# Kernel tuning notes

Hardware: AMD Instinct MI355X
Metric: run time of the kernel (lower is better)

The kernel has to match this reference:

```python
import jax, jax.numpy as jnp
import numpy as np

N_NODES = 50000
DEGREE = 32
NUM_FEATS = 128
NUM_HIDDEN = 128
NUM_LABELS = 40


def setup_inputs() -> dict:
    key = jax.random.key(0)
    k1, k2, k3, k4, k5, k6 = jax.random.split(key, 6)
    feats = jax.random.normal(k1, (N_NODES, NUM_FEATS), dtype=jnp.float32)
    neigh = jax.random.randint(k2, (N_NODES, DEGREE), 0, N_NODES, dtype=jnp.int32)
    batch = jnp.arange(N_NODES, dtype=jnp.int32)
    s1 = 1.0 / np.sqrt(2 * NUM_FEATS)
    s2 = 1.0 / np.sqrt(2 * NUM_HIDDEN)
    W1 = jax.random.uniform(k3, (2 * NUM_FEATS, NUM_HIDDEN), jnp.float32, -s1, s1)
    b1 = jax.random.uniform(k4, (NUM_HIDDEN,), jnp.float32, -s1, s1)
    W2 = jax.random.uniform(k5, (2 * NUM_HIDDEN, NUM_LABELS), jnp.float32, -s2, s2)
    b2 = jax.random.uniform(k6, (NUM_LABELS,), jnp.float32, -s2, s2)
    return {"feats": feats, "neigh": neigh, "batch": batch,
            "W1": W1, "b1": b1, "W2": W2, "b2": b2}


def reference(feats, neigh, batch, W1, b1, W2, b2):
    # Layer 1 (GraphConvolution with mean aggregator, relu; dropout in eval mode = identity).
    # Compute gc1 embeddings for ALL nodes once: identical math to the per-node
    # Python loop since the mean aggregator is deterministic.
    nbr_mean1 = jnp.take(feats, neigh, axis=0).mean(axis=1)          # [N, F]
    z1 = jnp.concatenate([feats, nbr_mean1], axis=-1)                # [N, 2F]
    h1 = jax.nn.relu(z1 @ W1 + b1)                                   # [N, H]
    # Layer 2 (no activation): concat self embedding with mean of neighbor embeddings.
    nbr_mean2 = jnp.take(h1, neigh[batch], axis=0).mean(axis=1)      # [B, H]
    z2 = jnp.concatenate([h1[batch], nbr_mean2], axis=-1)            # [B, 2H]
    return z2 @ W2 + b2                                              # [B, L]
```

## Files before the change

### kernel.cpp

```cpp
#include <hip/hip_runtime.h>
#include <hip/hip_bf16.h>

typedef __attribute__((ext_vector_type(8))) short short8;
typedef __attribute__((ext_vector_type(4))) float f32x4;

#define NFEAT 128
#define DEG 32
#define FSCALE 24.0f
#define FDEC (1.0f / (24.0f * 32.0f))
#define YSCALE 64.0f
#define YDEC (1.0f / (64.0f * 32.0f))

static __device__ __forceinline__ unsigned short f2bf(float f) {
    unsigned u = __float_as_uint(f);
    u += 0x7fffu + ((u >> 16) & 1u);
    return (unsigned short)(u >> 16);
}
static __device__ __forceinline__ int sxt8(unsigned x) {
    return (int)(signed char)(x & 0xffu);
}

__global__ void prep_all_kernel(const float* __restrict__ feats,
                                unsigned short* __restrict__ featsb,
                                unsigned* __restrict__ feats8,
                                const float* __restrict__ W1,
                                unsigned short* __restrict__ W1p,
                                const float* __restrict__ W2,
                                unsigned short* __restrict__ W2p,
                                int n4, int nPrepBlocks, int L) {
    int b = blockIdx.x;
    if (b < nPrepBlocks) {
        int i = b * 256 + threadIdx.x;
        if (i < n4) {
            float4 f = ((const float4*)feats)[i];
            ushort4 ob;
            ob.x = f2bf(f.x); ob.y = f2bf(f.y); ob.z = f2bf(f.z); ob.w = f2bf(f.w);
            ((ushort4*)featsb)[i] = ob;
            int a0 = max(-127, min(127, __float2int_rn(f.x * FSCALE)));
            int a1 = max(-127, min(127, __float2int_rn(f.y * FSCALE)));
            int a2 = max(-127, min(127, __float2int_rn(f.z * FSCALE)));
            int a3 = max(-127, min(127, __float2int_rn(f.w * FSCALE)));
            feats8[i] = (unsigned)(a0 & 0xff) | ((unsigned)(a1 & 0xff) << 8) |
                        ((unsigned)(a2 & 0xff) << 16) | ((unsigned)(a3 & 0xff) << 24);
        }
    } else if (b < nPrepBlocks + 128) {
        int t = (b - nPrepBlocks) * 256 + threadIdx.x;
        int j    = t & 7;
        int lane = (t >> 3) & 63;
        int ks   = (t >> 9) & 7;
        int nt   = t >> 12;
        int k    = ks * 32 + (lane >> 4) * 8 + j;
        int col  = nt * 16 + (lane & 15);
        W1p[t] = f2bf(W1[k * 128 + col]);
    } else {
        int t = (b - nPrepBlocks - 128) * 256 + threadIdx.x;
        if (t < 7 * 4 * 64 * 8) {
            int j    = t & 7;
            int lane = (t >> 3) & 63;
            int ks   = (t >> 9) & 3;
            int nt   = t >> 11;
            int k    = ks * 32 + (lane >> 4) * 8 + j;
            int p    = nt * 16 + (lane & 15);
            float v = 0.f;
            if (p < 48) { if (p < L) v = W2[k * L + p]; }
            else        { int cc = p - 48; if (cc < L) v = W2[(128 + k) * L + cc]; }
            W2p[t] = f2bf(v);
        }
    }
}

__global__ __launch_bounds__(256, 4) void layer1_fused_kernel(
    const unsigned short* __restrict__ tableb,
    const unsigned char* __restrict__ table8,
    const int* __restrict__ neigh,
    const unsigned short* __restrict__ W1p,
    const float* __restrict__ b1,
    const unsigned short* __restrict__ W2p,
    const float* __restrict__ b2,
    float* __restrict__ X2,
    signed char* __restrict__ Y2,
    int nRows, int L)
{
    __shared__ unsigned int z1[16 * 128];
    const int tid = threadIdx.x;
    const int w = tid >> 6;
    const int l = tid & 63;
    const int jg = l >> 3;
    const int c = l & 7;

    int srow = tid >> 4, sch = tid & 15;
    int sr = min(blockIdx.x * 16 + srow, nRows - 1);
    uint4 selfv = ((const uint4*)(tableb + (size_t)sr * NFEAT))[sch];

    const int r0 = blockIdx.x * 16 + w * 4;
    const int* nbp0 = neigh + (size_t)min(r0 + 0, nRows - 1) * DEG;
    const int* nbp1 = neigh + (size_t)min(r0 + 1, nRows - 1) * DEG;
    const int* nbp2 = neigh + (size_t)min(r0 + 2, nRows - 1) * DEG;
    const int* nbp3 = neigh + (size_t)min(r0 + 3, nRows - 1) * DEG;
    int i00 = nbp0[jg], i01 = nbp0[8 + jg], i02 = nbp0[16 + jg], i03 = nbp0[24 + jg];
    int i10 = nbp1[jg], i11 = nbp1[8 + jg], i12 = nbp1[16 + jg], i13 = nbp1[24 + jg];
    int i20 = nbp2[jg], i21 = nbp2[8 + jg], i22 = nbp2[16 + jg], i23 = nbp2[24 + jg];
    int i30 = nbp3[jg], i31 = nbp3[8 + jg], i32 = nbp3[16 + jg], i33 = nbp3[24 + jg];

    const char* tb8 = (const char*)table8;
    const size_t co = (size_t)(16 * c);
#define GLD16(j) (*(const uint4*)(tb8 + (size_t)(j) * 128 + co))
#define GATH4(A, a, b_, c_, d_) \
    uint4 A##0 = GLD16(a), A##1 = GLD16(b_), A##2 = GLD16(c_), A##3 = GLD16(d_);

    GATH4(vA, i00, i01, i02, i03)
    GATH4(vB, i10, i11, i12, i13)

    *(uint4*)((char*)z1 + srow * 512 + ((16 * sch) ^ ((srow & 7) << 4))) = selfv;

    GATH4(vC, i20, i21, i22, i23)

    int iacc[16];
#define UNPK(v)                                                        \
    {                                                                  \
        iacc[0]  += sxt8(v.x);       iacc[1]  += sxt8(v.x >> 8);       \
        iacc[2]  += sxt8(v.x >> 16); iacc[3]  += sxt8(v.x >> 24);      \
        iacc[4]  += sxt8(v.y);       iacc[5]  += sxt8(v.y >> 8);       \
        iacc[6]  += sxt8(v.y >> 16); iacc[7]  += sxt8(v.y >> 24);      \
        iacc[8]  += sxt8(v.z);       iacc[9]  += sxt8(v.z >> 8);       \
        iacc[10] += sxt8(v.z >> 16); iacc[11] += sxt8(v.z >> 24);      \
        iacc[12] += sxt8(v.w);       iacc[13] += sxt8(v.w >> 8);       \
        iacc[14] += sxt8(v.w >> 16); iacc[15] += sxt8(v.w >> 24);      \
    }
#define CONSUME16(A, rowi)                                                        \
    {                                                                             \
        _Pragma("unroll") for (int k = 0; k < 16; ++k) iacc[k] = 0;               \
        UNPK(A##0) UNPK(A##1) UNPK(A##2) UNPK(A##3)                               \
        _Pragma("unroll") for (int k = 0; k < 16; ++k) iacc[k] += __shfl_xor(iacc[k], 8);  \
        _Pragma("unroll") for (int k = 0; k < 16; ++k) iacc[k] += __shfl_xor(iacc[k], 16); \
        _Pragma("unroll") for (int k = 0; k < 16; ++k) iacc[k] += __shfl_xor(iacc[k], 32); \
        if (jg == 0) {                                                            \
            int row = w * 4 + rowi;                                               \
            int swz = (row & 7) << 4;                                             \
            uint4 m0, m1;                                                         \
            unsigned* mw0 = (unsigned*)&m0;                                       \
            unsigned* mw1 = (unsigned*)&m1;                                       \
            _Pragma("unroll") for (int k = 0; k < 4; ++k) {                       \
                mw0[k] = ((unsigned)f2bf((float)iacc[2 * k + 1] * FDEC) << 16) |  \
                         (unsigned)f2bf((float)iacc[2 * k] * FDEC);               \
                mw1[k] = ((unsigned)f2bf((float)iacc[2 * k + 9] * FDEC) << 16) |  \
                         (unsigned)f2bf((float)iacc[2 * k + 8] * FDEC);           \
            }                                                                     \
            *(uint4*)((char*)z1 + row * 512 + ((256 + 32 * c) ^ swz)) = m0;       \
            *(uint4*)((char*)z1 + row * 512 + ((256 + 32 * c + 16) ^ swz)) = m1;  \
        }                                                                         \
    }

    CONSUME16(vA, 0)
    GATH4(vD, i30, i31, i32, i33)
    CONSUME16(vB, 1)
    CONSUME16(vC, 2)
    CONSUME16(vD, 3)
#undef GLD16
#undef GATH4
#undef UNPK
#undef CONSUME16
    __syncthreads();

    f32x4 macc0 = (f32x4){0.f,0.f,0.f,0.f}, macc1 = (f32x4){0.f,0.f,0.f,0.f};
    {
        const int arow = l & 15;
        const int aswz = (arow & 7) << 4;
        const char* zbase = (const char*)z1 + arow * 512;
#pragma unroll
        for (int ks = 0; ks < 8; ++ks) {
            int kb = (ks * 64 + ((l >> 4) * 16)) ^ aswz;
            short8 a = *(const short8*)(zbase + kb);
            short8 b0 = *(const short8*)(W1p + ((size_t)((w * 2 + 0) * 8 + ks) * 64 + l) * 8);
            short8 b1f = *(const short8*)(W1p + ((size_t)((w * 2 + 1) * 8 + ks) * 64 + l) * 8);
            macc0 = __builtin_amdgcn_mfma_f32_16x16x32_bf16(a, b0, macc0, 0, 0, 0);
            macc1 = __builtin_amdgcn_mfma_f32_16x16x32_bf16(a, b1f, macc1, 0, 0, 0);
        }
    }
    __syncthreads();

#pragma unroll
    for (int tt = 0; tt < 2; ++tt) {
        int col = (w * 2 + tt) * 16 + (l & 15);
        float bv = b1[col];
        f32x4 m = tt ? macc1 : macc0;
#pragma unroll
        for (int r2 = 0; r2 < 4; ++r2) {
            int row = (l >> 4) * 4 + r2;
            float v = fmaxf(m[r2] + bv, 0.f);
            int byte = row * 256 + ((col * 2) ^ ((row & 7) << 4));
            *(unsigned short*)((char*)z1 + byte) = f2bf(v);
        }
    }
    __syncthreads();

    f32x4 acc2a = (f32x4){0.f,0.f,0.f,0.f}, acc2b = (f32x4){0.f,0.f,0.f,0.f};
    {
        const int arow = l & 15;
        const int aswz = (arow & 7) << 4;
        const char* hb = (const char*)z1 + arow * 256;
        const int ntA = w, ntB = 4 + w;
#pragma unroll
        for (int ks2 = 0; ks2 < 4; ++ks2) {
            short8 a = *(const short8*)(hb + ((ks2 * 64 + ((l >> 4) * 16)) ^ aswz));
            short8 bA = *(const short8*)(W2p + ((size_t)(ntA * 4 + ks2) * 64 + l) * 8);
            acc2a = __builtin_amdgcn_mfma_f32_16x16x32_bf16(a, bA, acc2a, 0, 0, 0);
            if (ntB < 7) {
                short8 bB = *(const short8*)(W2p + ((size_t)(ntB * 4 + ks2) * 64 + l) * 8);
                acc2b = __builtin_amdgcn_mfma_f32_16x16x32_bf16(a, bB, acc2b, 0, 0, 0);
            }
        }
    }

#pragma unroll
    for (int part = 0; part < 2; ++part) {
        int nt = part ? (4 + w) : w;
        if (nt >= 7) continue;
        f32x4 av = part ? acc2b : acc2a;
        int col = nt * 16 + (l & 15);
#pragma unroll
        for (int r2 = 0; r2 < 4; ++r2) {
            int row = blockIdx.x * 16 + (l >> 4) * 4 + r2;
            if (row >= nRows) continue;
            float v = av[r2];
            if (col < 48) {
                if (col < L) X2[(size_t)row * L + col] = v + b2[col];
            } else {
                int q = max(-127, min(127, __float2int_rn(v * YSCALE)));
                Y2[(size_t)row * 64 + (col - 48)] = (signed char)q;
            }
        }
    }
}

__global__ __launch_bounds__(256) void agg2_kernel(
    const float* __restrict__ X2,
    const unsigned char* __restrict__ Y2,
    const int* __restrict__ neigh,
    const int* __restrict__ batch,
    float* __restrict__ out,
    int nRows, int L)
{
    const int tid = threadIdx.x, w = tid >> 6, l = tid & 63;
    const int jg = l >> 3;
    const int c = l & 7;

    const int r0 = blockIdx.x * 16 + w * 4;
    int s[4];
    const int* nb[4];
#pragma unroll
    for (int rr = 0; rr < 4; ++rr) {
        int rc = min(r0 + rr, nRows - 1);
        s[rr] = batch[rc];
        nb[rr] = neigh + (size_t)s[rr] * DEG;
    }
    const char* yb = (const char*)Y2;
    const size_t co = (size_t)(8 * c);
#define YLD(j) (*(const uint2*)(yb + (size_t)(j) * 64 + co))
    uint2 v0[4], v1[4], v2[4], v3[4];
#pragma unroll
    for (int rr = 0; rr < 4; ++rr) {
        v0[rr] = YLD(nb[rr][jg]);
        v1[rr] = YLD(nb[rr][8 + jg]);
        v2[rr] = YLD(nb[rr][16 + jg]);
        v3[rr] = YLD(nb[rr][24 + jg]);
    }
#undef YLD

#pragma unroll
    for (int rr = 0; rr < 4; ++rr) {
        int iacc[8];
#pragma unroll
        for (int k = 0; k < 8; ++k) iacc[k] = 0;
#pragma unroll
        for (int q = 0; q < 4; ++q) {
            uint2 v = (q == 0) ? v0[rr] : (q == 1) ? v1[rr] : (q == 2) ? v2[rr] : v3[rr];
            unsigned x = v.x, y = v.y;
            iacc[0] += sxt8(x);       iacc[1] += sxt8(x >> 8);
            iacc[2] += sxt8(x >> 16); iacc[3] += sxt8(x >> 24);
            iacc[4] += sxt8(y);       iacc[5] += sxt8(y >> 8);
            iacc[6] += sxt8(y >> 16); iacc[7] += sxt8(y >> 24);
        }
#pragma unroll
        for (int k = 0; k < 8; ++k) {
            iacc[k] += __shfl_xor(iacc[k], 8);
            iacc[k] += __shfl_xor(iacc[k], 16);
            iacc[k] += __shfl_xor(iacc[k], 32);
        }
        int r = r0 + rr;
        if (jg == 0 && 8 * c < L && r < nRows) {
#pragma unroll
            for (int hv = 0; hv < 2; ++hv) {
                int colb = 8 * c + 4 * hv;
                if (colb < L) {
                    float4 xv = *(const float4*)(X2 + (size_t)s[rr] * L + colb);
                    float4 o;
                    o.x = xv.x + (float)iacc[4 * hv + 0] * YDEC;
                    o.y = xv.y + (float)iacc[4 * hv + 1] * YDEC;
                    o.z = xv.z + (float)iacc[4 * hv + 2] * YDEC;
                    o.w = xv.w + (float)iacc[4 * hv + 3] * YDEC;
                    *(float4*)(out + (size_t)r * L + colb) = o;
                }
            }
        }
    }
}

extern "C" void kernel_launch(void* const* d_in, const int* in_sizes, int n_in,
                              void* d_out, int out_size, void* d_ws, size_t ws_size,
                              hipStream_t stream) {
    const float* feats = (const float*)d_in[0];
    const int*   neigh = (const int*)d_in[1];
    const int*   batch = (const int*)d_in[2];
    const float* W1    = (const float*)d_in[3];
    const float* b1    = (const float*)d_in[4];
    const float* W2    = (const float*)d_in[5];
    const float* b2    = (const float*)d_in[6];

    const int N = in_sizes[0] / NFEAT;
    const int B = in_sizes[2];
    const int L = in_sizes[6];

    char* ws = (char*)d_ws;
    size_t off = 0;
    unsigned short* featsb = (unsigned short*)(ws + off); off += (size_t)N * NFEAT * 2;
    float*          X2     = (float*)(ws + off);          off += (size_t)N * L * 4;
    signed char*    Y2     = (signed char*)(ws + off);    off += (size_t)N * 64;
    unsigned char*  feats8 = (unsigned char*)(ws + off);  off += (size_t)N * NFEAT;
    unsigned short* W1p    = (unsigned short*)(ws + off); off += 8 * 8 * 64 * 8 * 2;
    unsigned short* W2p    = (unsigned short*)(ws + off); off += 7 * 4 * 64 * 8 * 2;

    int n4 = N * NFEAT / 4;
    int nPrepBlocks = (n4 + 255) / 256;
    int totalBlocks = nPrepBlocks + 128 + 56;
    prep_all_kernel<<<totalBlocks, 256, 0, stream>>>(
        feats, featsb, (unsigned*)feats8, W1, W1p, W2, W2p, n4, nPrepBlocks, L);

    layer1_fused_kernel<<<(N + 15) / 16, 256, 0, stream>>>(
        featsb, feats8, neigh, W1p, b1, W2p, b2, X2, Y2, N, L);

    agg2_kernel<<<(B + 15) / 16, 256, 0, stream>>>(
        X2, (const unsigned char*)Y2, neigh, batch, (float*)d_out, B, L);
}
```

Measured before the change: 148.2 us.

## Use 32-row blocks, packed int16 neighbor sums, separate h1 LDS buffer

```diff
diff --git a/kernel.cpp b/kernel.cpp
--- a/kernel.cpp
+++ b/kernel.cpp
@@ -3,6 +3,7 @@
 
 typedef __attribute__((ext_vector_type(8))) short short8;
 typedef __attribute__((ext_vector_type(4))) float f32x4;
+typedef __attribute__((ext_vector_type(2))) short s16x2;
 
 #define NFEAT 128
 #define DEG 32
@@ -18,6 +19,11 @@
 }
 static __device__ __forceinline__ int sxt8(unsigned x) {
     return (int)(signed char)(x & 0xffu);
+}
+static __device__ __forceinline__ s16x2 shfl_pk(s16x2 v, int m) {
+    int x = __builtin_bit_cast(int, v);
+    x = __shfl_xor(x, m);
+    return __builtin_bit_cast(s16x2, x);
 }
 
 __global__ void prep_all_kernel(const float* __restrict__ feats,
@@ -69,7 +75,7 @@
     }
 }
 
-__global__ __launch_bounds__(256, 4) void layer1_fused_kernel(
+__global__ __launch_bounds__(512, 8) void layer1_fused_kernel(
     const unsigned short* __restrict__ tableb,
     const unsigned char* __restrict__ table8,
     const int* __restrict__ neigh,
@@ -81,7 +87,8 @@
     signed char* __restrict__ Y2,
     int nRows, int L)
 {
-    __shared__ unsigned int z1[16 * 128];
+    __shared__ unsigned int z1[32 * 128];
+    __shared__ unsigned int h1s[32 * 68];
     const int tid = threadIdx.x;
     const int w = tid >> 6;
     const int l = tid & 63;
@@ -89,10 +96,10 @@
     const int c = l & 7;
 
     int srow = tid >> 4, sch = tid & 15;
-    int sr = min(blockIdx.x * 16 + srow, nRows - 1);
+    int sr = min(blockIdx.x * 32 + srow, nRows - 1);
     uint4 selfv = ((const uint4*)(tableb + (size_t)sr * NFEAT))[sch];
 
-    const int r0 = blockIdx.x * 16 + w * 4;
+    const int r0 = blockIdx.x * 32 + w * 4;
     const int* nbp0 = neigh + (size_t)min(r0 + 0, nRows - 1) * DEG;
     const int* nbp1 = neigh + (size_t)min(r0 + 1, nRows - 1) * DEG;
     const int* nbp2 = neigh + (size_t)min(r0 + 2, nRows - 1) * DEG;
@@ -115,94 +122,98 @@
 
     GATH4(vC, i20, i21, i22, i23)
 
-    int iacc[16];
-#define UNPK(v)                                                        \
-    {                                                                  \
-        iacc[0]  += sxt8(v.x);       iacc[1]  += sxt8(v.x >> 8);       \
-        iacc[2]  += sxt8(v.x >> 16); iacc[3]  += sxt8(v.x >> 24);      \
-        iacc[4]  += sxt8(v.y);       iacc[5]  += sxt8(v.y >> 8);       \
-        iacc[6]  += sxt8(v.y >> 16); iacc[7]  += sxt8(v.y >> 24);      \
-        iacc[8]  += sxt8(v.z);       iacc[9]  += sxt8(v.z >> 8);       \
-        iacc[10] += sxt8(v.z >> 16); iacc[11] += sxt8(v.z >> 24);      \
-        iacc[12] += sxt8(v.w);       iacc[13] += sxt8(v.w >> 8);       \
-        iacc[14] += sxt8(v.w >> 16); iacc[15] += sxt8(v.w >> 24);      \
-    }
-#define CONSUME16(A, rowi)                                                        \
-    {                                                                             \
-        _Pragma("unroll") for (int k = 0; k < 16; ++k) iacc[k] = 0;               \
-        UNPK(A##0) UNPK(A##1) UNPK(A##2) UNPK(A##3)                               \
-        _Pragma("unroll") for (int k = 0; k < 16; ++k) iacc[k] += __shfl_xor(iacc[k], 8);  \
-        _Pragma("unroll") for (int k = 0; k < 16; ++k) iacc[k] += __shfl_xor(iacc[k], 16); \
-        _Pragma("unroll") for (int k = 0; k < 16; ++k) iacc[k] += __shfl_xor(iacc[k], 32); \
-        if (jg == 0) {                                                            \
-            int row = w * 4 + rowi;                                               \
-            int swz = (row & 7) << 4;                                             \
-            uint4 m0, m1;                                                         \
-            unsigned* mw0 = (unsigned*)&m0;                                       \
-            unsigned* mw1 = (unsigned*)&m1;                                       \
-            _Pragma("unroll") for (int k = 0; k < 4; ++k) {                       \
-                mw0[k] = ((unsigned)f2bf((float)iacc[2 * k + 1] * FDEC) << 16) |  \
-                         (unsigned)f2bf((float)iacc[2 * k] * FDEC);               \
-                mw1[k] = ((unsigned)f2bf((float)iacc[2 * k + 9] * FDEC) << 16) |  \
-                         (unsigned)f2bf((float)iacc[2 * k + 8] * FDEC);           \
-            }                                                                     \
-            *(uint4*)((char*)z1 + row * 512 + ((256 + 32 * c) ^ swz)) = m0;       \
-            *(uint4*)((char*)z1 + row * 512 + ((256 + 32 * c + 16) ^ swz)) = m1;  \
-        }                                                                         \
-    }
-
-    CONSUME16(vA, 0)
+#define UNPK_PK(vd, d)                                                        \
+    {                                                                         \
+        unsigned _v = (vd);                                                   \
+        e[d] += (__builtin_bit_cast(s16x2, (unsigned)(_v << 8)) >> 8);        \
+        o[d] += (__builtin_bit_cast(s16x2, _v) >> 8);                         \
+    }
+#define CONSUME_PK(A, rowi)                                                          \
+    {                                                                                \
+        uint4 q0 = A##0, q1 = A##1, q2 = A##2, q3 = A##3;                            \
+        s16x2 e[4] = {(s16x2)0, (s16x2)0, (s16x2)0, (s16x2)0};                       \
+        s16x2 o[4] = {(s16x2)0, (s16x2)0, (s16x2)0, (s16x2)0};                       \
+        UNPK_PK(q0.x, 0) UNPK_PK(q0.y, 1) UNPK_PK(q0.z, 2) UNPK_PK(q0.w, 3)          \
+        UNPK_PK(q1.x, 0) UNPK_PK(q1.y, 1) UNPK_PK(q1.z, 2) UNPK_PK(q1.w, 3)          \
+        UNPK_PK(q2.x, 0) UNPK_PK(q2.y, 1) UNPK_PK(q2.z, 2) UNPK_PK(q2.w, 3)          \
+        UNPK_PK(q3.x, 0) UNPK_PK(q3.y, 1) UNPK_PK(q3.z, 2) UNPK_PK(q3.w, 3)          \
+        _Pragma("unroll") for (int d = 0; d < 4; ++d) {                              \
+            e[d] += shfl_pk(e[d], 8);  o[d] += shfl_pk(o[d], 8);                     \
+            e[d] += shfl_pk(e[d], 16); o[d] += shfl_pk(o[d], 16);                    \
+            e[d] += shfl_pk(e[d], 32); o[d] += shfl_pk(o[d], 32);                    \
+        }                                                                            \
+        if (jg == 0) {                                                               \
+            int row = w * 4 + rowi;                                                  \
+            int swz = (row & 7) << 4;                                                \
+            uint4 m0, m1;                                                            \
+            unsigned* mw0 = (unsigned*)&m0;                                          \
+            unsigned* mw1 = (unsigned*)&m1;                                          \
+            _Pragma("unroll") for (int d = 0; d < 2; ++d) {                          \
+                mw0[2*d]   = ((unsigned)f2bf((float)o[d].x * FDEC) << 16) |          \
+                             (unsigned)f2bf((float)e[d].x * FDEC);                   \
+                mw0[2*d+1] = ((unsigned)f2bf((float)o[d].y * FDEC) << 16) |          \
+                             (unsigned)f2bf((float)e[d].y * FDEC);                   \
+                mw1[2*d]   = ((unsigned)f2bf((float)o[d+2].x * FDEC) << 16) |        \
+                             (unsigned)f2bf((float)e[d+2].x * FDEC);                 \
+                mw1[2*d+1] = ((unsigned)f2bf((float)o[d+2].y * FDEC) << 16) |        \
+                             (unsigned)f2bf((float)e[d+2].y * FDEC);                 \
+            }                                                                        \
+            *(uint4*)((char*)z1 + row * 512 + ((256 + 32 * c) ^ swz)) = m0;          \
+            *(uint4*)((char*)z1 + row * 512 + ((256 + 32 * c + 16) ^ swz)) = m1;     \
+        }                                                                            \
+    }
+
+    CONSUME_PK(vA, 0)
     GATH4(vD, i30, i31, i32, i33)
-    CONSUME16(vB, 1)
-    CONSUME16(vC, 2)
-    CONSUME16(vD, 3)
+    CONSUME_PK(vB, 1)
+    CONSUME_PK(vC, 2)
+    CONSUME_PK(vD, 3)
 #undef GLD16
 #undef GATH4
-#undef UNPK
-#undef CONSUME16
+#undef UNPK_PK
+#undef CONSUME_PK
     __syncthreads();
 
     f32x4 macc0 = (f32x4){0.f,0.f,0.f,0.f}, macc1 = (f32x4){0.f,0.f,0.f,0.f};
+    const int rt = w >> 2;
+    const int nt0 = (w & 3) * 2;
     {
-        const int arow = l & 15;
+        const int arow = rt * 16 + (l & 15);
         const int aswz = (arow & 7) << 4;
         const char* zbase = (const char*)z1 + arow * 512;
 #pragma unroll
         for (int ks = 0; ks < 8; ++ks) {
             int kb = (ks * 64 + ((l >> 4) * 16)) ^ aswz;
             short8 a = *(const short8*)(zbase + kb);
-            short8 b0 = *(const short8*)(W1p + ((size_t)((w * 2 + 0) * 8 + ks) * 64 + l) * 8);
-            short8 b1f = *(const short8*)(W1p + ((size_t)((w * 2 + 1) * 8 + ks) * 64 + l) * 8);
+            short8 b0 = *(const short8*)(W1p + ((size_t)((nt0 + 0) * 8 + ks) * 64 + l) * 8);
+            short8 b1f = *(const short8*)(W1p + ((size_t)((nt0 + 1) * 8 + ks) * 64 + l) * 8);
             macc0 = __builtin_amdgcn_mfma_f32_16x16x32_bf16(a, b0, macc0, 0, 0, 0);
             macc1 = __builtin_amdgcn_mfma_f32_16x16x32_bf16(a, b1f, macc1, 0, 0, 0);
         }
     }
-    __syncthreads();
 
 #pragma unroll
     for (int tt = 0; tt < 2; ++tt) {
-        int col = (w * 2 + tt) * 16 + (l & 15);
+        int col = (nt0 + tt) * 16 + (l & 15);
         float bv = b1[col];
         f32x4 m = tt ? macc1 : macc0;
 #pragma unroll
         for (int r2 = 0; r2 < 4; ++r2) {
-            int row = (l >> 4) * 4 + r2;
+            int row = rt * 16 + (l >> 4) * 4 + r2;
             float v = fmaxf(m[r2] + bv, 0.f);
-            int byte = row * 256 + ((col * 2) ^ ((row & 7) << 4));
-            *(unsigned short*)((char*)z1 + byte) = f2bf(v);
+            *(unsigned short*)((char*)h1s + row * 272 + col * 2) = f2bf(v);
         }
     }
     __syncthreads();
 
     f32x4 acc2a = (f32x4){0.f,0.f,0.f,0.f}, acc2b = (f32x4){0.f,0.f,0.f,0.f};
+    const int ntA = w & 3, ntB = 4 + (w & 3);
     {
-        const int arow = l & 15;
-        const int aswz = (arow & 7) << 4;
-        const char* hb = (const char*)z1 + arow * 256;
-        const int ntA = w, ntB = 4 + w;
+        const int arow = rt * 16 + (l & 15);
+        const char* hb = (const char*)h1s + arow * 272;
 #pragma unroll
         for (int ks2 = 0; ks2 < 4; ++ks2) {
-            short8 a = *(const short8*)(hb + ((ks2 * 64 + ((l >> 4) * 16)) ^ aswz));
+            short8 a = *(const short8*)(hb + ks2 * 64 + ((l >> 4) * 16));
             short8 bA = *(const short8*)(W2p + ((size_t)(ntA * 4 + ks2) * 64 + l) * 8);
             acc2a = __builtin_amdgcn_mfma_f32_16x16x32_bf16(a, bA, acc2a, 0, 0, 0);
             if (ntB < 7) {
@@ -214,13 +225,13 @@
 
 #pragma unroll
     for (int part = 0; part < 2; ++part) {
-        int nt = part ? (4 + w) : w;
+        int nt = part ? ntB : ntA;
         if (nt >= 7) continue;
         f32x4 av = part ? acc2b : acc2a;
         int col = nt * 16 + (l & 15);
 #pragma unroll
         for (int r2 = 0; r2 < 4; ++r2) {
-            int row = blockIdx.x * 16 + (l >> 4) * 4 + r2;
+            int row = blockIdx.x * 32 + rt * 16 + (l >> 4) * 4 + r2;
             if (row >= nRows) continue;
             float v = av[r2];
             if (col < 48) {
@@ -336,7 +347,7 @@
     prep_all_kernel<<<totalBlocks, 256, 0, stream>>>(
         feats, featsb, (unsigned*)feats8, W1, W1p, W2, W2p, n4, nPrepBlocks, L);
 
-    layer1_fused_kernel<<<(N + 15) / 16, 256, 0, stream>>>(
+    layer1_fused_kernel<<<(N + 31) / 32, 512, 0, stream>>>(
         featsb, feats8, neigh, W1p, b1, W2p, b2, X2, Y2, N, L);
 
     agg2_kernel<<<(B + 15) / 16, 256, 0, stream>>>(
```

Result: slower. 160.9 us (+8.6%).
